# Kernel tuning notes

Measured on AMD Instinct MI355X. Metric: run time of the kernel, lower is better.

The kernel has to match this reference:

```python
import jax, jax.numpy as jnp
import numpy as np

N, L, D = 64, 510, 768
L1, K, OUT = 128, 20, 300
EPS = 1e-5


def _make_spans(key, n, n_spans, max_len):
    ks, kl = jax.random.split(key)
    starts = jnp.sort(jax.random.randint(ks, (n, n_spans), 0, max_len - 4), axis=1)
    lens = jax.random.randint(kl, (n, n_spans), 1, 5)
    ends = jnp.minimum(starts + lens, max_len)
    return starts.astype(jnp.int32), ends.astype(jnp.int32)


def setup_inputs() -> dict:
    key = jax.random.key(0)
    ks = jax.random.split(key, 10)
    t1 = jax.random.normal(ks[0], (N, L, D), jnp.float32)
    encoded_know = jax.random.normal(ks[1], (N, L, D), jnp.float32)
    span_starts, span_ends = _make_spans(ks[2], N, L1, L)
    know_span_starts, know_span_ends = _make_spans(ks[3], N, K, L)
    # padding masks: True = masked; guarantee >=1 valid entry per row
    valid1 = jax.random.randint(ks[4], (N,), L1 // 2, L1 + 1)
    key_padding_mask = jnp.arange(L1)[None, :] >= valid1[:, None]
    validk = jax.random.randint(ks[5], (N,), 5, K + 1)
    key_padding_mask_know = jnp.arange(K)[None, :] >= validk[:, None]
    W_lin = jax.random.normal(ks[6], (OUT, D), jnp.float32) * 0.02
    b_lin = jnp.zeros((OUT,), jnp.float32)
    gamma = jnp.ones((OUT,), jnp.float32)
    beta = jnp.zeros((OUT,), jnp.float32)
    W_score = jax.random.normal(ks[7], (1, OUT), jnp.float32) * 0.02
    b_score = jnp.zeros((1,), jnp.float32)
    return dict(t1=t1, encoded_know=encoded_know,
                span_starts=span_starts, span_ends=span_ends,
                key_padding_mask=key_padding_mask,
                know_span_starts=know_span_starts, know_span_ends=know_span_ends,
                key_padding_mask_know=key_padding_mask_know,
                W_lin=W_lin, b_lin=b_lin, gamma=gamma, beta=beta,
                W_score=W_score, b_score=b_score)


def _span_mean(x, starts, ends):
    # x: (N,L,D); spans [s,e) -> mean via inclusive-scan difference (one pass)
    n, l, d = x.shape
    cs = jnp.concatenate([jnp.zeros((n, 1, d), x.dtype), jnp.cumsum(x, axis=1)], axis=1)
    gather = lambda idx: jnp.take_along_axis(cs, idx[:, :, None].astype(jnp.int32), axis=1)
    sums = gather(ends) - gather(starts)  # (N, n_spans, D)
    lens = jnp.maximum(ends - starts, 1).astype(x.dtype)[:, :, None]
    return sums / lens


def _layernorm(x, g, b):
    m = jnp.mean(x, axis=-1, keepdims=True)
    v = jnp.mean(jnp.square(x - m), axis=-1, keepdims=True)
    return (x - m) * jax.lax.rsqrt(v + EPS) * g + b


def reference(t1, encoded_know, span_starts, span_ends, key_padding_mask,
              know_span_starts, know_span_ends, key_padding_mask_know,
              W_lin, b_lin, gamma, beta, W_score, b_score):
    lam = 1.0

    def branch(x, s, e, mask):
        pooled = _span_mean(x, s, e)                       # ragged segment mean
        h = _layernorm(pooled @ W_lin.T + b_lin, gamma, beta)
        sc = (h @ W_score.T + b_score)[..., 0]             # (N, n_spans)
        sc = jnp.where(mask, -jnp.inf, sc)                 # masked_fill
        return h, jax.nn.softmax(sc * lam, axis=1)

    h1, s1 = branch(t1, span_starts, span_ends, key_padding_mask)
    hk, sk = branch(encoded_know, know_span_starts, know_span_ends, key_padding_mask_know)
    score = jnp.broadcast_to(s1[:, :, None], h1.shape)     # repeat to (N,L1,OUT)
    return h1, score, hk, sk
```

## Files before the change

### kernel.cpp

```cpp
#include <hip/hip_runtime.h>
#include <hip/hip_bf16.h>
#include <stdint.h>

#define NB    64
#define LSEQ  510
#define DIN   768
#define L1S   128
#define KS    20
#define OUTF  300
#define NPAD  320
#define EPSL  1e-5f

#define M1    (NB * L1S)
#define MK    (NB * KS)
#define MT    (M1 + MK)

#define OFF_H1    0
#define OFF_SCORE (M1 * OUTF)
#define OFF_HK    (2 * M1 * OUTF)
#define OFF_SK    (OFF_HK + MK * OUTF)

#define WS_FLAG    0
#define WS_SCORES  64
#define WS_WBF     81920

typedef short  short8_t  __attribute__((ext_vector_type(8)));
typedef float  float4v_t __attribute__((ext_vector_type(4)));
typedef unsigned short ushort4_t __attribute__((ext_vector_type(4)));

#define SA_STRIDE 776
#define SC_STRIDE 324
#define LDS_BYTES 41984

__device__ inline bool mask_at(const void* m, int idx, int flag) {
    switch (flag) {
        case 1:  return ((const unsigned char*)m)[idx] != 0;
        case 2:  return ((const float*)m)[idx] != 0.0f;
        case 3:  return ((const unsigned short*)m)[idx] != 0;
        default: return ((const int*)m)[idx] != 0;
    }
}

__global__ __launch_bounds__(256)
void prep_kernel(const unsigned int* __restrict__ p, int* __restrict__ flag,
                 const float* __restrict__ W, unsigned short* __restrict__ Wb) {
    if (blockIdx.x == 0) {
        __shared__ int f_bf16, f_f32, f_other;
        if (threadIdx.x == 0) { f_bf16 = 0; f_f32 = 0; f_other = 0; }
        __syncthreads();
        for (int i = threadIdx.x; i < 2048; i += blockDim.x) {
            unsigned int v = p[i];
            if (v <= 1u) continue;
            if (v == 0x3F803F80u)       atomicOr(&f_bf16, 1);
            else if (v == 0x3F800000u)  atomicOr(&f_f32, 1);
            else                        atomicOr(&f_other, 1);
        }
        __syncthreads();
        if (threadIdx.x == 0) {
            int f = 0;
            if (f_bf16)       f = 3;
            else if (f_f32)   f = 2;
            else if (f_other) f = 1;
            *flag = f;
        }
        return;
    }
    int idx = (blockIdx.x - 1) * 256 + threadIdx.x;
    if (idx >= NPAD * DIN) return;
    int r = idx / DIN;
    float v = (r < OUTF) ? W[idx] : 0.f;
    __hip_bfloat16 b = __float2bfloat16(v);
    Wb[idx] = *(unsigned short*)&b;
}

__global__ __launch_bounds__(640, 5)
void fused_gemm_kernel(const float* __restrict__ t1,
                       const float* __restrict__ know,
                       const int* __restrict__ s1s, const int* __restrict__ s1e,
                       const int* __restrict__ kss, const int* __restrict__ kse,
                       const unsigned short* __restrict__ Wb,
                       const float* __restrict__ bias,
                       const float* __restrict__ gamma,
                       const float* __restrict__ beta,
                       const float* __restrict__ Wsc,
                       const float* __restrict__ bsc,
                       float* __restrict__ out,
                       float* __restrict__ scores) {
    __shared__ unsigned long long lds_raw[LDS_BYTES / 8];
    unsigned short* sA   = (unsigned short*)lds_raw;
    int*   sSrc = (int*)  ((char*)lds_raw + 16 * 1552);
    int*   sLen = (int*)  ((char*)lds_raw + 16 * 1552 + 64);
    float* sInv = (float*)((char*)lds_raw + 16 * 1552 + 128);

    const int tid = threadIdx.x;
    const int R0  = blockIdx.x * 16;
    const bool isk = (R0 >= M1);

    if (tid < 16) {
        int g = R0 + tid;
        int s, e, n;
        if (!isk) { n = g >> 7;          s = s1s[g];      e = s1e[g]; }
        else      { int gg = g - M1; n = gg / KS; s = kss[gg]; e = kse[gg]; }
        if (s < 0) s = 0;
        if (e > LSEQ) e = LSEQ;
        int len = e - s; if (len < 1) len = 1;
        sSrc[tid] = n * (LSEQ * (DIN / 4)) + s * (DIN / 4);
        sLen[tid] = len;
        sInv[tid] = 1.0f / (float)len;
    }
    __syncthreads();

    const float4* src4 = (const float4*)(isk ? know : t1);
    for (int t = tid; t < 16 * 192; t += 640) {
        int sp = t / 192;
        int c4 = t - sp * 192;
        const float4* p = src4 + sSrc[sp] + c4;
        int len = sLen[sp];
        const float4 z = {0.f, 0.f, 0.f, 0.f};
        float4 v0 = p[0];
        float4 v1 = z, v2 = z, v3 = z;
        if (len > 1) v1 = p[1 * 192];
        if (len > 2) v2 = p[2 * 192];
        if (len > 3) v3 = p[3 * 192];
        float4 acc;
        acc.x = (v0.x + v1.x) + (v2.x + v3.x);
        acc.y = (v0.y + v1.y) + (v2.y + v3.y);
        acc.z = (v0.z + v1.z) + (v2.z + v3.z);
        acc.w = (v0.w + v1.w) + (v2.w + v3.w);
        for (int r = 4; r < len; ++r) {
            float4 v = p[r * 192];
            acc.x += v.x; acc.y += v.y; acc.z += v.z; acc.w += v.w;
        }
        float inv = sInv[sp];
        __hip_bfloat16 b0 = __float2bfloat16(acc.x * inv);
        __hip_bfloat16 b1 = __float2bfloat16(acc.y * inv);
        __hip_bfloat16 b2 = __float2bfloat16(acc.z * inv);
        __hip_bfloat16 b3 = __float2bfloat16(acc.w * inv);
        ushort4_t pk;
        pk.x = *(unsigned short*)&b0; pk.y = *(unsigned short*)&b1;
        pk.z = *(unsigned short*)&b2; pk.w = *(unsigned short*)&b3;
        *(ushort4_t*)(sA + sp * SA_STRIDE + c4 * 4) = pk;
    }
    __syncthreads();

    const int wave = tid >> 6;
    const int lane = tid & 63;
    const int quad = lane >> 4;
    const int l16  = lane & 15;
    const int cg   = wave % 5;
    const int kh   = wave / 5;

    const unsigned short* sArow = sA + l16 * SA_STRIDE + quad * 8 + kh * 384;
    const unsigned short* bb = Wb + (size_t)(cg * 64 + l16) * DIN + quad * 8 + kh * 384;

    float4v_t acc0 = {0.f, 0.f, 0.f, 0.f};
    float4v_t acc1 = {0.f, 0.f, 0.f, 0.f};
    float4v_t acc2 = {0.f, 0.f, 0.f, 0.f};
    float4v_t acc3 = {0.f, 0.f, 0.f, 0.f};

#pragma unroll 4
    for (int k0 = 0; k0 < 384; k0 += 32) {
        short8_t a  = *(const short8_t*)(sArow + k0);
        short8_t b0 = *(const short8_t*)(bb + 0 * 16 * DIN + k0);
        short8_t b1 = *(const short8_t*)(bb + 1 * 16 * DIN + k0);
        short8_t b2 = *(const short8_t*)(bb + 2 * 16 * DIN + k0);
        short8_t b3 = *(const short8_t*)(bb + 3 * 16 * DIN + k0);
        acc0 = __builtin_amdgcn_mfma_f32_16x16x32_bf16(a, b0, acc0, 0, 0, 0);
        acc1 = __builtin_amdgcn_mfma_f32_16x16x32_bf16(a, b1, acc1, 0, 0, 0);
        acc2 = __builtin_amdgcn_mfma_f32_16x16x32_bf16(a, b2, acc2, 0, 0, 0);
        acc3 = __builtin_amdgcn_mfma_f32_16x16x32_bf16(a, b3, acc3, 0, 0, 0);
    }

    __syncthreads();
    float* sC = (float*)lds_raw;
#pragma unroll
    for (int i = 0; i < 4; ++i) {
        int r = (kh * 16 + quad * 4 + i) * SC_STRIDE + cg * 64 + l16;
        sC[r +  0] = acc0[i];
        sC[r + 16] = acc1[i];
        sC[r + 32] = acc2[i];
        sC[r + 48] = acc3[i];
    }
    __syncthreads();

    if (wave < 8) {
        const float bs0 = bsc[0];
#pragma unroll
        for (int rr = 0; rr < 2; ++rr) {
            const int r = wave * 2 + rr;
            const int g = R0 + r;
            float tv[5];
            float s = 0.f;
#pragma unroll
            for (int m = 0; m < 5; ++m) {
                int c = lane + 64 * m;
                float v = 0.f;
                if (c < OUTF)
                    v = sC[r * SC_STRIDE + c] + sC[(16 + r) * SC_STRIDE + c] + bias[c];
                tv[m] = v; s += v;
            }
#pragma unroll
            for (int off = 32; off > 0; off >>= 1) s += __shfl_xor(s, off, 64);
            const float mean = s * (1.0f / OUTF);
            float vs = 0.f;
#pragma unroll
            for (int m = 0; m < 5; ++m) {
                int c = lane + 64 * m;
                float d = (c < OUTF) ? (tv[m] - mean) : 0.f;
                vs += d * d;
            }
#pragma unroll
            for (int off = 32; off > 0; off >>= 1) vs += __shfl_xor(vs, off, 64);
            const float rstd = rsqrtf(vs * (1.0f / OUTF) + EPSL);

            const size_t off0 = isk ? (size_t)OFF_HK + (size_t)(g - M1) * OUTF
                                    : (size_t)g * OUTF;
            float sc = 0.f;
#pragma unroll
            for (int m = 0; m < 5; ++m) {
                int c = lane + 64 * m;
                if (c < OUTF) {
                    float h = (tv[m] - mean) * rstd * gamma[c] + beta[c];
                    out[off0 + c] = h;
                    sc += h * Wsc[c];
                }
            }
#pragma unroll
            for (int off = 32; off > 0; off >>= 1) sc += __shfl_xor(sc, off, 64);
            if (lane == 0) scores[g] = sc + bs0;
        }
    }
}

__global__ __launch_bounds__(128)
void softmax_bcast_kernel(const float* __restrict__ scores,
                          const void* __restrict__ m1,
                          const void* __restrict__ mk,
                          const int* __restrict__ flagp,
                          float* __restrict__ out) {
    const int flag = *flagp;
    const int b = blockIdx.x;
    const int tid = threadIdx.x;
    const int lane = tid & 63;

    if (b < NB * 5) {
        __shared__ float sprob[L1S];
        const int n = b / 5;
        const int chunk = b - n * 5;
        if (tid < 64) {
            float v0 = scores[n * L1S + lane];
            float v1 = scores[n * L1S + lane + 64];
            if (mask_at(m1, n * L1S + lane, flag))      v0 = -INFINITY;
            if (mask_at(m1, n * L1S + lane + 64, flag)) v1 = -INFINITY;
            float mx = fmaxf(v0, v1);
#pragma unroll
            for (int off = 32; off > 0; off >>= 1) mx = fmaxf(mx, __shfl_xor(mx, off, 64));
            float e0 = __expf(v0 - mx);
            float e1 = __expf(v1 - mx);
            float s = e0 + e1;
#pragma unroll
            for (int off = 32; off > 0; off >>= 1) s += __shfl_xor(s, off, 64);
            float inv = 1.0f / s;
            sprob[lane]      = e0 * inv;
            sprob[lane + 64] = e1 * inv;
        }
        __syncthreads();
        float* dst = out + (size_t)OFF_SCORE + (size_t)n * (L1S * OUTF);
        const int cbase = chunk * 7680;
#pragma unroll
        for (int i = 0; i < 15; ++i) {
            int e0i = cbase + (i * 128 + tid) * 4;
            float4 v;
            v.x = sprob[(e0i + 0) / OUTF];
            v.y = sprob[(e0i + 1) / OUTF];
            v.z = sprob[(e0i + 2) / OUTF];
            v.w = sprob[(e0i + 3) / OUTF];
            *(float4*)(dst + e0i) = v;
        }
    } else {
        const int n = (b - NB * 5) * 2 + (tid >> 6);
        float v = -INFINITY;
        if (lane < KS) {
            v = scores[M1 + n * KS + lane];
            if (mask_at(mk, n * KS + lane, flag)) v = -INFINITY;
        }
        float mx = v;
#pragma unroll
        for (int off = 32; off > 0; off >>= 1) mx = fmaxf(mx, __shfl_xor(mx, off, 64));
        float e = (lane < KS) ? __expf(v - mx) : 0.f;
        float s = e;
#pragma unroll
        for (int off = 32; off > 0; off >>= 1) s += __shfl_xor(s, off, 64);
        if (lane < KS) out[(size_t)OFF_SK + n * KS + lane] = e / s;
    }
}

extern "C" void kernel_launch(void* const* d_in, const int* in_sizes, int n_in,
                              void* d_out, int out_size, void* d_ws, size_t ws_size,
                              hipStream_t stream) {
    const float* t1   = (const float*)d_in[0];
    const float* know = (const float*)d_in[1];
    const int* s1s = (const int*)d_in[2];
    const int* s1e = (const int*)d_in[3];
    const void* m1 = d_in[4];
    const int* kss = (const int*)d_in[5];
    const int* kse = (const int*)d_in[6];
    const void* mk = d_in[7];
    const float* Wl  = (const float*)d_in[8];
    const float* bl  = (const float*)d_in[9];
    const float* gm  = (const float*)d_in[10];
    const float* bt  = (const float*)d_in[11];
    const float* Wsc = (const float*)d_in[12];
    const float* bsc = (const float*)d_in[13];
    float* out = (float*)d_out;

    char* ws = (char*)d_ws;
    int*            flag   = (int*)(ws + WS_FLAG);
    float*          scores = (float*)(ws + WS_SCORES);
    unsigned short* Wb     = (unsigned short*)(ws + WS_WBF);

    prep_kernel<<<1 + (NPAD * DIN + 255) / 256, 256, 0, stream>>>(
        (const unsigned int*)m1, flag, Wl, Wb);
    fused_gemm_kernel<<<MT / 16, 640, 0, stream>>>(t1, know, s1s, s1e, kss, kse,
                                                   Wb, bl, gm, bt, Wsc, bsc,
                                                   out, scores);
    softmax_bcast_kernel<<<NB * 5 + NB / 2, 128, 0, stream>>>(scores, m1, mk,
                                                              flag, out);
}
```

Before: 259.9 us.

## Split span pooling into separate kernel feeding a bf16 GEMM kernel

Splits the fused pool+GEMM kernel into two kernels. A pooling kernel computes span means with float4 loads spread across many threads and writes bf16 pooled rows to workspace. A GEMM kernel then loads those rows into LDS and runs the MFMA plus LayerNorm epilogue. The aim is better memory parallelism for the gather-heavy pooling, paid for with an extra kernel launch and a round trip of the pooled data through global memory. The old fused path is kept as a fallback when the workspace is too small.

```diff
diff --git a/kernel.cpp b/kernel.cpp
--- a/kernel.cpp
+++ b/kernel.cpp
@@ -23,10 +23,13 @@
 #define WS_FLAG    0
 #define WS_SCORES  64
 #define WS_WBF     81920
+#define WS_POOLED  1048576
+#define WS_NEEDED  (WS_POOLED + (size_t)MT * DIN * 2)
 
 typedef short  short8_t  __attribute__((ext_vector_type(8)));
 typedef float  float4v_t __attribute__((ext_vector_type(4)));
 typedef unsigned short ushort4_t __attribute__((ext_vector_type(4)));
+typedef unsigned short ushort8_t __attribute__((ext_vector_type(8)));
 
 #define SA_STRIDE 776
 #define SC_STRIDE 324
@@ -71,6 +74,169 @@
     float v = (r < OUTF) ? W[idx] : 0.f;
     __hip_bfloat16 b = __float2bfloat16(v);
     Wb[idx] = *(unsigned short*)&b;
+}
+
+__global__ __launch_bounds__(256)
+void pool_kernel(const float* __restrict__ t1, const float* __restrict__ know,
+                 const int* __restrict__ s1s, const int* __restrict__ s1e,
+                 const int* __restrict__ kss, const int* __restrict__ kse,
+                 unsigned short* __restrict__ pooled) {
+    const int idx = blockIdx.x * 256 + threadIdx.x;
+    const int g  = idx / 192;
+    const int c4 = idx - g * 192;
+    int s, e;
+    const float* src;
+    if (g < M1) {
+        s = s1s[g]; e = s1e[g];
+        src = t1 + (size_t)(g >> 7) * (LSEQ * DIN);
+    } else {
+        int gg = g - M1;
+        s = kss[gg]; e = kse[gg];
+        src = know + (size_t)(gg / KS) * (LSEQ * DIN);
+    }
+    if (s < 0) s = 0;
+    if (e > LSEQ) e = LSEQ;
+    int len = e - s; if (len < 1) len = 1;
+
+    const float4* p = (const float4*)src + s * 192 + c4;
+    const float4 z = {0.f, 0.f, 0.f, 0.f};
+    float4 v0 = p[0];
+    float4 v1 = z, v2 = z, v3 = z;
+    if (len > 1) v1 = p[1 * 192];
+    if (len > 2) v2 = p[2 * 192];
+    if (len > 3) v3 = p[3 * 192];
+    float4 acc;
+    acc.x = (v0.x + v1.x) + (v2.x + v3.x);
+    acc.y = (v0.y + v1.y) + (v2.y + v3.y);
+    acc.z = (v0.z + v1.z) + (v2.z + v3.z);
+    acc.w = (v0.w + v1.w) + (v2.w + v3.w);
+    for (int r = 4; r < len; ++r) {
+        float4 v = p[r * 192];
+        acc.x += v.x; acc.y += v.y; acc.z += v.z; acc.w += v.w;
+    }
+    const float inv = 1.0f / (float)len;
+    __hip_bfloat16 b0 = __float2bfloat16(acc.x * inv);
+    __hip_bfloat16 b1 = __float2bfloat16(acc.y * inv);
+    __hip_bfloat16 b2 = __float2bfloat16(acc.z * inv);
+    __hip_bfloat16 b3 = __float2bfloat16(acc.w * inv);
+    ushort4_t pk;
+    pk.x = *(unsigned short*)&b0; pk.y = *(unsigned short*)&b1;
+    pk.z = *(unsigned short*)&b2; pk.w = *(unsigned short*)&b3;
+    *(ushort4_t*)(pooled + (size_t)g * DIN + c4 * 4) = pk;
+}
+
+__global__ __launch_bounds__(640, 5)
+void gemm_kernel(const unsigned short* __restrict__ pooled,
+                 const unsigned short* __restrict__ Wb,
+                 const float* __restrict__ bias,
+                 const float* __restrict__ gamma,
+                 const float* __restrict__ beta,
+                 const float* __restrict__ Wsc,
+                 const float* __restrict__ bsc,
+                 float* __restrict__ out,
+                 float* __restrict__ scores) {
+    __shared__ unsigned long long lds_raw[LDS_BYTES / 8];
+    unsigned short* sA = (unsigned short*)lds_raw;
+
+    const int tid = threadIdx.x;
+    const int R0  = blockIdx.x * 16;
+    const bool isk = (R0 >= M1);
+
+    for (int t = tid; t < 16 * 96; t += 640) {
+        int sp = t / 96;
+        int c8 = t - sp * 96;
+        ushort8_t v = *(const ushort8_t*)(pooled + (size_t)(R0 + sp) * DIN + c8 * 8);
+        *(ushort8_t*)(sA + sp * SA_STRIDE + c8 * 8) = v;
+    }
+    __syncthreads();
+
+    const int wave = tid >> 6;
+    const int lane = tid & 63;
+    const int quad = lane >> 4;
+    const int l16  = lane & 15;
+    const int cg   = wave % 5;
+    const int kh   = wave / 5;
+
+    const unsigned short* sArow = sA + l16 * SA_STRIDE + quad * 8 + kh * 384;
+    const unsigned short* bb = Wb + (size_t)(cg * 64 + l16) * DIN + quad * 8 + kh * 384;
+
+    float4v_t acc0 = {0.f, 0.f, 0.f, 0.f};
+    float4v_t acc1 = {0.f, 0.f, 0.f, 0.f};
+    float4v_t acc2 = {0.f, 0.f, 0.f, 0.f};
+    float4v_t acc3 = {0.f, 0.f, 0.f, 0.f};
+
+#pragma unroll 4
+    for (int k0 = 0; k0 < 384; k0 += 32) {
+        short8_t a  = *(const short8_t*)(sArow + k0);
+        short8_t b0 = *(const short8_t*)(bb + 0 * 16 * DIN + k0);
+        short8_t b1 = *(const short8_t*)(bb + 1 * 16 * DIN + k0);
+        short8_t b2 = *(const short8_t*)(bb + 2 * 16 * DIN + k0);
+        short8_t b3 = *(const short8_t*)(bb + 3 * 16 * DIN + k0);
+        acc0 = __builtin_amdgcn_mfma_f32_16x16x32_bf16(a, b0, acc0, 0, 0, 0);
+        acc1 = __builtin_amdgcn_mfma_f32_16x16x32_bf16(a, b1, acc1, 0, 0, 0);
+        acc2 = __builtin_amdgcn_mfma_f32_16x16x32_bf16(a, b2, acc2, 0, 0, 0);
+        acc3 = __builtin_amdgcn_mfma_f32_16x16x32_bf16(a, b3, acc3, 0, 0, 0);
+    }
+
+    __syncthreads();
+    float* sC = (float*)lds_raw;
+#pragma unroll
+    for (int i = 0; i < 4; ++i) {
+        int r = (kh * 16 + quad * 4 + i) * SC_STRIDE + cg * 64 + l16;
+        sC[r +  0] = acc0[i];
+        sC[r + 16] = acc1[i];
+        sC[r + 32] = acc2[i];
+        sC[r + 48] = acc3[i];
+    }
+    __syncthreads();
+
+    if (wave < 8) {
+        const float bs0 = bsc[0];
+#pragma unroll
+        for (int rr = 0; rr < 2; ++rr) {
+            const int r = wave * 2 + rr;
+            const int g = R0 + r;
+            float tv[5];
+            float s = 0.f;
+#pragma unroll
+            for (int m = 0; m < 5; ++m) {
+                int c = lane + 64 * m;
+                float v = 0.f;
+                if (c < OUTF)
+                    v = sC[r * SC_STRIDE + c] + sC[(16 + r) * SC_STRIDE + c] + bias[c];
+                tv[m] = v; s += v;
+            }
+#pragma unroll
+            for (int off = 32; off > 0; off >>= 1) s += __shfl_xor(s, off, 64);
+            const float mean = s * (1.0f / OUTF);
+            float vs = 0.f;
+#pragma unroll
+            for (int m = 0; m < 5; ++m) {
+                int c = lane + 64 * m;
+                float d = (c < OUTF) ? (tv[m] - mean) : 0.f;
+                vs += d * d;
+            }
+#pragma unroll
+            for (int off = 32; off > 0; off >>= 1) vs += __shfl_xor(vs, off, 64);
+            const float rstd = rsqrtf(vs * (1.0f / OUTF) + EPSL);
+
+            const size_t off0 = isk ? (size_t)OFF_HK + (size_t)(g - M1) * OUTF
+                                    : (size_t)g * OUTF;
+            float sc = 0.f;
+#pragma unroll
+            for (int m = 0; m < 5; ++m) {
+                int c = lane + 64 * m;
+                if (c < OUTF) {
+                    float h = (tv[m] - mean) * rstd * gamma[c] + beta[c];
+                    out[off0 + c] = h;
+                    sc += h * Wsc[c];
+                }
+            }
+#pragma unroll
+            for (int off = 32; off > 0; off >>= 1) sc += __shfl_xor(sc, off, 64);
+            if (lane == 0) scores[g] = sc + bs0;
+        }
+    }
 }
 
 __global__ __launch_bounds__(640, 5)
@@ -318,12 +484,21 @@
     int*            flag   = (int*)(ws + WS_FLAG);
     float*          scores = (float*)(ws + WS_SCORES);
     unsigned short* Wb     = (unsigned short*)(ws + WS_WBF);
+    unsigned short* pooled = (unsigned short*)(ws + WS_POOLED);
 
     prep_kernel<<<1 + (NPAD * DIN + 255) / 256, 256, 0, stream>>>(
         (const unsigned int*)m1, flag, Wl, Wb);
-    fused_gemm_kernel<<<MT / 16, 640, 0, stream>>>(t1, know, s1s, s1e, kss, kse,
-                                                   Wb, bl, gm, bt, Wsc, bsc,
-                                                   out, scores);
+
+    if (ws_size >= WS_NEEDED) {
+        pool_kernel<<<(MT * 192) / 256, 256, 0, stream>>>(t1, know, s1s, s1e,
+                                                          kss, kse, pooled);
+        gemm_kernel<<<MT / 16, 640, 0, stream>>>(pooled, Wb, bl, gm, bt,
+                                                 Wsc, bsc, out, scores);
+    } else {
+        fused_gemm_kernel<<<MT / 16, 640, 0, stream>>>(t1, know, s1s, s1e,
+                                                       kss, kse, Wb, bl, gm,
+                                                       bt, Wsc, bsc, out, scores);
+    }
     softmax_bcast_kernel<<<NB * 5 + NB / 2, 128, 0, stream>>>(scores, m1, mk,
                                                               flag, out);
 }
```

Measured after the change: 268.6 us. +3.3%, slower.
